# Kernel optimization log

Hardware: AMD Instinct MI355X
Metric: run time of the kernel (lower is better)

## Reference

```python
import jax, jax.numpy as jnp
import numpy as np

EPS = 1e-8

def _fft_unit_proj(x):
    # Project each vector to unit magnitude in the Fourier domain (norm_kv=True).
    f = jnp.fft.fft(x, axis=-1)
    return jnp.real(jnp.fft.ifft(f / (jnp.abs(f) + EPS), axis=-1))

def _hrr_key_value_query(k, v, q, causal=True):
    # k, v, q: [B, S, D]
    k = _fft_unit_proj(k)
    v = _fft_unit_proj(v)
    # bind: circular convolution of key and value
    kv = jnp.real(jnp.fft.ifft(jnp.fft.fft(k, axis=-1) * jnp.fft.fft(v, axis=-1), axis=-1))
    # causal associative memory: running sum of bound pairs along sequence
    if causal:
        mem = jnp.cumsum(kv, axis=1)
    else:
        mem = jnp.broadcast_to(jnp.sum(kv, axis=1, keepdims=True), kv.shape)
    # unbind: circular correlation of memory with query
    out = jnp.real(jnp.fft.ifft(jnp.conj(jnp.fft.fft(q, axis=-1)) * jnp.fft.fft(mem, axis=-1), axis=-1))
    return out


def setup_inputs() -> dict:
    key = jax.random.key(0)
    ks = jax.random.split(key, 8)
    B, S, D = 2, 4096, 2048
    sc = 1.0 / np.sqrt(D).astype(np.float32)
    return {
        "hidden_states": jax.random.normal(ks[0], (B, S, D), jnp.float32),
        "base_output": jax.random.normal(ks[1], (B, S, D), jnp.float32),
        "Wq": jax.random.normal(ks[2], (D, D), jnp.float32) * sc,
        "bq": jnp.zeros((D,), jnp.float32),
        "Wk": jax.random.normal(ks[3], (D, D), jnp.float32) * sc,
        "bk": jnp.zeros((D,), jnp.float32),
        "Wv": jax.random.normal(ks[4], (D, D), jnp.float32) * sc,
        "bv": jnp.zeros((D,), jnp.float32),
        "gate": jax.random.normal(ks[5], (1,), jnp.float32) * 0.1,
    }


def reference(hidden_states, base_output, Wq, bq, Wk, bk, Wv, bv, gate):
    # Adapter q/k/v projections (nn.Linear uses y = x @ W.T + b)
    q = jnp.einsum('bsd,ed->bse', hidden_states, Wq) + bq
    k = jnp.einsum('bsd,ed->bse', hidden_states, Wk) + bk
    v = jnp.einsum('bsd,ed->bse', hidden_states, Wv) + bv
    adapter = _hrr_key_value_query(k, v, q, causal=True)
    return base_output + gate * adapter
```

## Files before the change

### kernel.cpp

```cpp
#include <hip/hip_runtime.h>
#include <math.h>

constexpr int D_DIM  = 2048;
constexpr int HALF_D = 1024;
constexpr int B_DIM  = 2;
constexpr int S_DIM  = 4096;
constexpr int NROW   = B_DIM * S_DIM;
constexpr int NCHUNK = 64;
constexpr int CHLEN  = S_DIM / NCHUNK;
constexpr float EPS_ = 1e-8f;

typedef __attribute__((ext_vector_type(8))) short  short8;
typedef __attribute__((ext_vector_type(8))) unsigned short ushort8;
typedef __attribute__((ext_vector_type(4))) float  f32x4;

__device__ __forceinline__ float2 mkf2(float x, float y){ float2 r; r.x=x; r.y=y; return r; }
__device__ __forceinline__ float2 cmulf(float2 a, float2 b){
  return mkf2(fmaf(a.x, b.x, -a.y*b.y), fmaf(a.x, b.y, a.y*b.x));
}
__device__ __forceinline__ unsigned short f2bf(float x){
  unsigned u = __float_as_uint(x);
  u += 0x7fff + ((u >> 16) & 1);
  return (unsigned short)(u >> 16);
}
__device__ __forceinline__ float bf2f(unsigned short h){
  return __uint_as_float(((unsigned)h) << 16);
}

__global__ __launch_bounds__(256)
void cvt_f32_bf16(const float* __restrict__ in, unsigned short* __restrict__ out, int n8)
{
  int i = blockIdx.x * 256 + threadIdx.x;
  if (i >= n8) return;
  const float4* p = (const float4*)in + (size_t)i * 2;
  float4 a = p[0], b = p[1];
  ushort8 o;
  o[0]=f2bf(a.x); o[1]=f2bf(a.y); o[2]=f2bf(a.z); o[3]=f2bf(a.w);
  o[4]=f2bf(b.x); o[5]=f2bf(b.y); o[6]=f2bf(b.z); o[7]=f2bf(b.w);
  *(ushort8*)(out + (size_t)i * 8) = o;
}

__global__ __launch_bounds__(512, 2)
void gemm_fused(const unsigned short* __restrict__ A,
                const unsigned short* __restrict__ Wc,
                const float* __restrict__ bq, const float* __restrict__ bk,
                const float* __restrict__ bv,
                float* __restrict__ qout, unsigned short* __restrict__ kvb)
{
  constexpr int K = 2048, NT = K / 32;
  __shared__ unsigned short lds[49152];
  const int tid  = threadIdx.x;
  const int wid  = tid >> 6, lane = tid & 63;
  const int wr   = wid >> 2, wc = wid & 3;

  int bid = blockIdx.x;
  int sw  = (bid & 7) * 96 + (bid >> 3);
  const int bm = (sw / 24) * 256, bn = (sw % 24) * 256;

  const int srow = tid >> 2;
  const int skc  = ((tid & 3) ^ ((tid >> 3) & 3)) * 8;
  const unsigned short* Ag = A  + (size_t)(bm + srow) * K + skc;
  const unsigned short* Bg = Wc + (size_t)(bn + srow) * K + skc;

  unsigned short* Abase = lds;
  unsigned short* Bbase = lds + 24576;
  const int stoff = wid * 512;

  const int fr  = lane & 15;
  const int sig = ((lane >> 4) ^ ((lane >> 1) & 3)) * 8;
  const int aro = (wr * 128 + fr) * 32 + sig;
  const int bro = (wc * 64 + fr) * 32 + sig;

  auto stA = [&](int kt, int b, int r) {
    __builtin_amdgcn_global_load_lds(
      (const __attribute__((address_space(1))) void*)(Ag + (size_t)r * 128 * K + kt * 32),
      (__attribute__((address_space(3))) void*)(Abase + b * 8192 + r * 4096 + stoff),
      16, 0, 0);
  };
  auto stB = [&](int kt, int b, int r) {
    __builtin_amdgcn_global_load_lds(
      (const __attribute__((address_space(1))) void*)(Bg + (size_t)r * 128 * K + kt * 32),
      (__attribute__((address_space(3))) void*)(Bbase + b * 8192 + r * 4096 + stoff),
      16, 0, 0);
  };

  f32x4 acc[8][4];
#pragma unroll
  for (int i = 0; i < 8; ++i)
#pragma unroll
    for (int j = 0; j < 4; ++j) acc[i][j] = (f32x4){0.f, 0.f, 0.f, 0.f};

  stA(0, 0, 0); stA(0, 0, 1); stB(0, 0, 0); stB(0, 0, 1);
  stA(1, 1, 0); stA(1, 1, 1); stB(1, 1, 0); stB(1, 1, 1);
  asm volatile("s_waitcnt vmcnt(4)" ::: "memory");
  __builtin_amdgcn_s_barrier();
  __builtin_amdgcn_sched_barrier(0);

  int c = 0;
#pragma unroll 1
  for (int kt = 0; kt < NT; ++kt) {
    const unsigned short* Ab = Abase + c * 8192;
    const unsigned short* Bb = Bbase + c * 8192;
    int nb = c + 2; if (nb >= 3) nb -= 3;
    const bool st = (kt < NT - 2);

    if (st) { stA(kt + 2, nb, 0); stA(kt + 2, nb, 1); }
    short8 af0[4], bfr[4];
#pragma unroll
    for (int i = 0; i < 4; ++i) af0[i] = *(const short8*)(Ab + aro + i * 512);
#pragma unroll
    for (int j = 0; j < 4; ++j) bfr[j] = *(const short8*)(Bb + bro + j * 512);
    __builtin_amdgcn_s_barrier();
    asm volatile("s_waitcnt lgkmcnt(0)" ::: "memory");
    __builtin_amdgcn_sched_barrier(0);
    __builtin_amdgcn_s_setprio(1);
#pragma unroll
    for (int i = 0; i < 4; ++i)
#pragma unroll
      for (int j = 0; j < 4; ++j)
        acc[i][j] = __builtin_amdgcn_mfma_f32_16x16x32_bf16(af0[i], bfr[j], acc[i][j], 0, 0, 0);
    __builtin_amdgcn_s_setprio(0);
    __builtin_amdgcn_s_barrier();

    if (st) { stB(kt + 2, nb, 0); stB(kt + 2, nb, 1); }
    short8 af1[4];
#pragma unroll
    for (int i = 0; i < 4; ++i) af1[i] = *(const short8*)(Ab + aro + 2048 + i * 512);
    __builtin_amdgcn_s_barrier();
    asm volatile("s_waitcnt lgkmcnt(0)" ::: "memory");
    __builtin_amdgcn_sched_barrier(0);
    __builtin_amdgcn_s_setprio(1);
#pragma unroll
    for (int i = 0; i < 4; ++i)
#pragma unroll
      for (int j = 0; j < 4; ++j)
        acc[4 + i][j] = __builtin_amdgcn_mfma_f32_16x16x32_bf16(af1[i], bfr[j], acc[4 + i][j], 0, 0, 0);
    __builtin_amdgcn_s_setprio(0);
    if (st)                 asm volatile("s_waitcnt vmcnt(4)" ::: "memory");
    else if (kt == NT - 2)  asm volatile("s_waitcnt vmcnt(0)" ::: "memory");
    __builtin_amdgcn_s_barrier();
    c = (c == 2) ? 0 : c + 1;
  }

  const int seg = bn >> 11;
  const float* bp = (seg == 0) ? bq : (seg == 1) ? bk : bv;
  float bias_j[4];
#pragma unroll
  for (int j = 0; j < 4; ++j)
    bias_j[j] = bp[(bn + wc * 64 + j * 16 + fr) & 2047];
  const int er = (lane >> 4) * 4;
  const int kvoff = (seg == 2) ? 2048 : 0;
#pragma unroll
  for (int I = 0; I < 8; ++I) {
    int row = bm + wr * 128 + I * 16 + er;
#pragma unroll
    for (int j = 0; j < 4; ++j) {
      int col = (bn + wc * 64 + j * 16 + fr) & 2047;
#pragma unroll
      for (int r = 0; r < 4; ++r) {
        float val = acc[I][j][r] + bias_j[j];
        if (seg == 0)
          qout[(size_t)(row + r) * 2048 + col] = val;
        else
          kvb[(size_t)(row + r) * 4096 + kvoff + col] = f2bf(val);
      }
    }
  }
}

__device__ __forceinline__ int XS(int i){ return i ^ (((i >> 5) ^ (i >> 10)) & 31); }
__device__ __forceinline__ int TS(int i){ return i ^ ((i >> 5) & 31); }

__device__ __forceinline__ float2 mulmi(float2 w){ return mkf2(w.y, -w.x); }
__device__ __forceinline__ float2 mulw8(float2 w){
  const float c = 0.70710678118654752f;
  return mkf2(c * (w.x + w.y), c * (w.y - w.x));
}
__device__ __forceinline__ void bfly(float2& a, float2& b, float2 w){
  float2 v = cmulf(w, b);
  b = mkf2(a.x - v.x, a.y - v.y);
  a = mkf2(a.x + v.x, a.y + v.y);
}
__device__ __forceinline__ void bflyc(float2& a, float2& b, float2 w){
  float2 d = mkf2(a.x - b.x, a.y - b.y);
  a = mkf2(a.x + b.x, a.y + b.y);
  b = mkf2(fmaf(d.x, w.x, d.y * w.y), fmaf(d.y, w.x, -d.x * w.y));
}

__device__ __forceinline__ void fwd8(float2 e[8], float2 wA, float2 wB0, float2 wC0){
  bfly(e[0], e[1], wA); bfly(e[2], e[3], wA); bfly(e[4], e[5], wA); bfly(e[6], e[7], wA);
  float2 wB1 = mulmi(wB0);
  bfly(e[0], e[2], wB0); bfly(e[1], e[3], wB1); bfly(e[4], e[6], wB0); bfly(e[5], e[7], wB1);
  float2 wC1 = mulw8(wC0), wC2 = mulmi(wC0), wC3 = mulmi(wC1);
  bfly(e[0], e[4], wC0); bfly(e[1], e[5], wC1); bfly(e[2], e[6], wC2); bfly(e[3], e[7], wC3);
}
__device__ __forceinline__ void inv8(float2 e[8], float2 wA, float2 wB0, float2 wC0){
  float2 wC1 = mulw8(wC0), wC2 = mulmi(wC0), wC3 = mulmi(wC1);
  bflyc(e[0], e[4], wC0); bflyc(e[1], e[5], wC1); bflyc(e[2], e[6], wC2); bflyc(e[3], e[7], wC3);
  float2 wB1 = mulmi(wB0);
  bflyc(e[0], e[2], wB0); bflyc(e[1], e[3], wB1); bflyc(e[4], e[6], wB0); bflyc(e[5], e[7], wB1);
  bflyc(e[0], e[1], wA); bflyc(e[2], e[3], wA); bflyc(e[4], e[5], wA); bflyc(e[6], e[7], wA);
}

__device__ __forceinline__ float2 twld(const float* twr, const float* twi, int i){
  int s = TS(i);
  return mkf2(twr[s], twi[s]);
}

__device__ void fft_fwd(float2* X, const float* twr, const float* twi, int t)
{
  const float2 one = mkf2(1.f, 0.f);
  {
    int b = 8 * t;
    float2 e[8];
#pragma unroll
    for (int r = 0; r < 8; ++r) e[r] = X[XS(b + r)];
    fwd8(e, one, one, one);
#pragma unroll
    for (int r = 0; r < 8; ++r) X[XS(b + r)] = e[r];
  }
  __syncthreads();
  {
    int u = t >> 5, b = 64 * (t & 31) + u;
    float2 e[8];
#pragma unroll
    for (int r = 0; r < 8; ++r) e[r] = X[XS(b + 8 * r)];
    fwd8(e, twld(twr,twi,128*u), twld(twr,twi,64*u), twld(twr,twi,32*u));
#pragma unroll
    for (int r = 0; r < 8; ++r) X[XS(b + 8 * r)] = e[r];
  }
  __syncthreads();
  {
    int u = t & 63, b = 512 * (t >> 6) + u;
    float2 e[8];
#pragma unroll
    for (int r = 0; r < 8; ++r) e[r] = X[XS(b + 64 * r)];
    fwd8(e, twld(twr,twi,16*u), twld(twr,twi,8*u), twld(twr,twi,4*u));
#pragma unroll
    for (int r = 0; r < 8; ++r) X[XS(b + 64 * r)] = e[r];
  }
  __syncthreads();
#pragma unroll
  for (int h = 0; h < 2; ++h) {
    int u = t + 256 * h;
    float2 f[4];
#pragma unroll
    for (int r = 0; r < 4; ++r) f[r] = X[XS(u + 512 * r)];
    float2 wA = twld(twr,twi,2*u), wB0 = twld(twr,twi,u), wB1 = mulmi(wB0);
    bfly(f[0], f[1], wA);  bfly(f[2], f[3], wA);
    bfly(f[0], f[2], wB0); bfly(f[1], f[3], wB1);
#pragma unroll
    for (int r = 0; r < 4; ++r) X[XS(u + 512 * r)] = f[r];
  }
  __syncthreads();
}

__device__ void fft_inv(float2* X, const float* twr, const float* twi, int t)
{
  const float2 one = mkf2(1.f, 0.f);
#pragma unroll
  for (int h = 0; h < 2; ++h) {
    int u = t + 256 * h;
    float2 f[4];
#pragma unroll
    for (int r = 0; r < 4; ++r) f[r] = X[XS(u + 512 * r)];
    float2 wA = twld(twr,twi,2*u), wB0 = twld(twr,twi,u), wB1 = mulmi(wB0);
    bflyc(f[0], f[2], wB0); bflyc(f[1], f[3], wB1);
    bflyc(f[0], f[1], wA);  bflyc(f[2], f[3], wA);
#pragma unroll
    for (int r = 0; r < 4; ++r) X[XS(u + 512 * r)] = f[r];
  }
  __syncthreads();
  {
    int u = t & 63, b = 512 * (t >> 6) + u;
    float2 e[8];
#pragma unroll
    for (int r = 0; r < 8; ++r) e[r] = X[XS(b + 64 * r)];
    inv8(e, twld(twr,twi,16*u), twld(twr,twi,8*u), twld(twr,twi,4*u));
#pragma unroll
    for (int r = 0; r < 8; ++r) X[XS(b + 64 * r)] = e[r];
  }
  __syncthreads();
  {
    int u = t >> 5, b = 64 * (t & 31) + u;
    float2 e[8];
#pragma unroll
    for (int r = 0; r < 8; ++r) e[r] = X[XS(b + 8 * r)];
    inv8(e, twld(twr,twi,128*u), twld(twr,twi,64*u), twld(twr,twi,32*u));
#pragma unroll
    for (int r = 0; r < 8; ++r) X[XS(b + 8 * r)] = e[r];
  }
  __syncthreads();
  {
    int b = 8 * t;
    float2 e[8];
#pragma unroll
    for (int r = 0; r < 8; ++r) e[r] = X[XS(b + r)];
    inv8(e, one, one, one);
#pragma unroll
    for (int r = 0; r < 8; ++r) X[XS(b + r)] = e[r];
  }
  __syncthreads();
}

__global__ __launch_bounds__(256)
void twiddle_init(float2* __restrict__ twg)
{
  int i = blockIdx.x * 256 + threadIdx.x;
  if (i < HALF_D) {
    float sv, cv;
    sincosf(-6.283185307179586f * (float)i / (float)D_DIM, &sv, &cv);
    twg[i] = mkf2(cv, sv);
  }
}

__global__ __launch_bounds__(256)
void fftkv_kernel(unsigned short* __restrict__ kvb, const float2* __restrict__ twg)
{
  __shared__ float2 X[D_DIM];
  __shared__ float twr[HALF_D], twi[HALF_D];
  const int t = threadIdx.x;
  const size_t row = blockIdx.x;
  const unsigned short* kvrow = kvb + row * 4096;

  for (int i = t; i < HALF_D; i += 256) {
    float2 w = twg[i]; int s = TS(i); twr[s] = w.x; twi[s] = w.y;
  }
  for (int i = t; i < D_DIM; i += 256) {
    int p = __brev((unsigned)i) >> 21;
    X[XS(p)] = mkf2(bf2f(kvrow[i]), bf2f(kvrow[2048 + i]));
  }
  __syncthreads();
  fft_fwd(X, twr, twi, t);

  float2* outp = (float2*)(kvb + row * 4096);
  for (int d = t; d < HALF_D; d += 256) {
    float2 p;
    if (d == 0) {
      float2 z0 = X[XS(0)], zn = X[XS(HALF_D)];
      float k0 = z0.x, v0 = z0.y, kn = zn.x, vn = zn.y;
      float p0 = (k0 / (fabsf(k0) + EPS_)) * (v0 / (fabsf(v0) + EPS_));
      float pn = (kn / (fabsf(kn) + EPS_)) * (vn / (fabsf(vn) + EPS_));
      p = mkf2(p0, pn);
    } else {
      float2 A = X[XS(d)];
      float2 Bc = X[XS(D_DIM - d)];
      float2 Bj = mkf2(Bc.x, -Bc.y);
      float2 Fk = mkf2(0.5f * (A.x + Bj.x), 0.5f * (A.y + Bj.y));
      float2 tt = mkf2(0.5f * (A.x - Bj.x), 0.5f * (A.y - Bj.y));
      float2 Fv = mkf2(tt.y, -tt.x);
      float sa = 1.f / (sqrtf(Fk.x*Fk.x + Fk.y*Fk.y) + EPS_);
      float sb = 1.f / (sqrtf(Fv.x*Fv.x + Fv.y*Fv.y) + EPS_);
      p = cmulf(Fk, Fv);
      float sc = sa * sb;
      p.x *= sc; p.y *= sc;
    }
    outp[d] = p;
  }
}

__global__ __launch_bounds__(256)
void scan_partial(const float2* __restrict__ kv, float2* __restrict__ part)
{
  int gid = blockIdx.x * 256 + threadIdx.x;
  int d = gid & (HALF_D - 1);
  int chunk = (gid >> 10) & (NCHUNK - 1);
  int b = gid >> 16;
  const float2* p = kv + ((size_t)(b * S_DIM + chunk * CHLEN) * HALF_D) + d;
  float2 acc = mkf2(0.f, 0.f);
  for (int s = 0; s < CHLEN; ++s) {
    float2 v = p[(size_t)s * HALF_D];
    acc.x += v.x; acc.y += v.y;
  }
  part[gid] = acc;
}

__global__ __launch_bounds__(256)
void scan_offsets(float2* __restrict__ part)
{
  int gid = blockIdx.x * 256 + threadIdx.x;
  int d = gid & (HALF_D - 1);
  int b = gid >> 10;
  float2* p = part + (size_t)b * (NCHUNK * HALF_D) + d;
  float2 acc = mkf2(0.f, 0.f);
  for (int c = 0; c < NCHUNK; ++c) {
    float2 v = p[(size_t)c * HALF_D];
    p[(size_t)c * HALF_D] = acc;
    acc.x += v.x; acc.y += v.y;
  }
}

__global__ __launch_bounds__(256)
void scan_apply(float2* __restrict__ kv, const float2* __restrict__ part)
{
  int gid = blockIdx.x * 256 + threadIdx.x;
  int d = gid & (HALF_D - 1);
  int chunk = (gid >> 10) & (NCHUNK - 1);
  int b = gid >> 16;
  float2* p = kv + ((size_t)(b * S_DIM + chunk * CHLEN) * HALF_D) + d;
  float2 acc = part[gid];
  for (int s = 0; s < CHLEN; ++s) {
    float2 v = p[(size_t)s * HALF_D];
    acc.x += v.x; acc.y += v.y;
    p[(size_t)s * HALF_D] = acc;
  }
}

__global__ __launch_bounds__(256)
void final_kernel(float* __restrict__ qo, const float2* __restrict__ mem,
                  const float* __restrict__ base, const float* __restrict__ gate,
                  const float2* __restrict__ twg)
{
  __shared__ float2 X[D_DIM];
  __shared__ float twr[HALF_D], twi[HALF_D];
  const int t = threadIdx.x;
  const size_t row = blockIdx.x;
  float* qrow = qo + row * D_DIM;
  const float2* mrow = mem + row * HALF_D;

  for (int i = t; i < HALF_D; i += 256) {
    float2 w = twg[i]; int s = TS(i); twr[s] = w.x; twi[s] = w.y;
  }
  for (int i = t; i < D_DIM; i += 256) {
    int p = __brev((unsigned)i) >> 21;
    X[XS(p)] = mkf2(qrow[i], 0.f);
  }
  __syncthreads();
  fft_fwd(X, twr, twi, t);

  for (int d = t; d < HALF_D; d += 256) {
    if (d == 0) {
      float2 fm = mrow[0];
      float2 f0 = X[XS(0)], f1 = X[XS(HALF_D)];
      X[XS(0)]      = mkf2(f0.x * fm.x, -f0.y * fm.x);
      X[XS(HALF_D)] = mkf2(f1.x * fm.y, -f1.y * fm.y);
    } else {
      float2 fm = mrow[d];
      float2 fq = X[XS(d)];
      X[XS(d)] = mkf2(fq.x*fm.x + fq.y*fm.y, fq.x*fm.y - fq.y*fm.x);
      float2 f2 = X[XS(D_DIM - d)];
      X[XS(D_DIM - d)] = mkf2(f2.x*fm.x - f2.y*fm.y, -f2.x*fm.y - f2.y*fm.x);
    }
  }
  __syncthreads();
  fft_inv(X, twr, twi, t);

  const float gv = gate[0] * (1.f / (float)D_DIM);
  const float* brow = base + row * D_DIM;
  for (int i = t; i < D_DIM; i += 256) {
    int p = __brev((unsigned)i) >> 21;
    qrow[i] = brow[i] + gv * X[XS(p)].x;
  }
}

extern "C" void kernel_launch(void* const* d_in, const int* in_sizes, int n_in,
                              void* d_out, int out_size, void* d_ws, size_t ws_size,
                              hipStream_t stream)
{
  const float* hs   = (const float*)d_in[0];
  const float* base = (const float*)d_in[1];
  const float* Wq   = (const float*)d_in[2];
  const float* bq   = (const float*)d_in[3];
  const float* Wk   = (const float*)d_in[4];
  const float* bk   = (const float*)d_in[5];
  const float* Wv   = (const float*)d_in[6];
  const float* bv   = (const float*)d_in[7];
  const float* gate = (const float*)d_in[8];
  float* out  = (float*)d_out;

  char* ws = (char*)d_ws;
  unsigned short* hsb = (unsigned short*)ws;
  unsigned short* wqb = (unsigned short*)(ws + 33554432);
  unsigned short* wkb = wqb + (size_t)D_DIM * D_DIM;
  unsigned short* wvb = wkb + (size_t)D_DIM * D_DIM;
  unsigned short* kvb = (unsigned short*)(ws + 58720256);
  float2* part = (float2*)(ws + 58720256 + 67108864);
  float2* twg  = (float2*)ws;

  {
    int n8 = (NROW * D_DIM) / 8;
    cvt_f32_bf16<<<n8 / 256, 256, 0, stream>>>(hs, hsb, n8);
    int w8 = (D_DIM * D_DIM) / 8;
    cvt_f32_bf16<<<w8 / 256, 256, 0, stream>>>(Wq, wqb, w8);
    cvt_f32_bf16<<<w8 / 256, 256, 0, stream>>>(Wk, wkb, w8);
    cvt_f32_bf16<<<w8 / 256, 256, 0, stream>>>(Wv, wvb, w8);
  }

  gemm_fused<<<768, 512, 0, stream>>>(hsb, wqb, bq, bk, bv, out, kvb);

  twiddle_init<<<4, 256, 0, stream>>>(twg);

  fftkv_kernel<<<NROW, 256, 0, stream>>>(kvb, twg);

  scan_partial<<<(B_DIM * NCHUNK * HALF_D) / 256, 256, 0, stream>>>(
      (const float2*)kvb, part);
  scan_offsets<<<(B_DIM * HALF_D) / 256, 256, 0, stream>>>(part);
  scan_apply<<<(B_DIM * NCHUNK * HALF_D) / 256, 256, 0, stream>>>(
      (float2*)kvb, part);

  final_kernel<<<NROW, 256, 0, stream>>>(out, (const float2*)kvb, base, gate, twg);
}
```

Measured before the change: 433.3 us.

## Store q and frequency-domain kv in bf16, vectorize scans, retile GEMM to 256x128

The GEMM now writes q as bf16 instead of fp32. The fftkv kernel packs its complex spectrum output into bf16 pairs. The scan and final kernels read and write these bf16 buffers with 16-byte vectorized accesses and fp32 accumulators. The GEMM is retiled from 256x256 blocks of 512 threads to 256x128 blocks of 256 threads, with the LDS staging resized to match. The aim is to halve intermediate memory traffic in the bandwidth-bound scan and FFT stages, but the running-sum memory rounded to bf16 adds accuracy risk, and the scan kernels now launch only 128 blocks.

Result: faster. 404.4 us (-6.7%).

```diff
diff --git a/kernel.cpp b/kernel.cpp
--- a/kernel.cpp
+++ b/kernel.cpp
@@ -40,22 +40,22 @@
   *(ushort8*)(out + (size_t)i * 8) = o;
 }
 
-__global__ __launch_bounds__(512, 2)
+__global__ __launch_bounds__(256, 2)
 void gemm_fused(const unsigned short* __restrict__ A,
                 const unsigned short* __restrict__ Wc,
                 const float* __restrict__ bq, const float* __restrict__ bk,
                 const float* __restrict__ bv,
-                float* __restrict__ qout, unsigned short* __restrict__ kvb)
+                unsigned short* __restrict__ qb, unsigned short* __restrict__ kvb)
 {
   constexpr int K = 2048, NT = K / 32;
-  __shared__ unsigned short lds[49152];
+  __shared__ unsigned short lds[36864];
   const int tid  = threadIdx.x;
   const int wid  = tid >> 6, lane = tid & 63;
-  const int wr   = wid >> 2, wc = wid & 3;
+  const int wr   = wid >> 1, wc = wid & 1;
 
   int bid = blockIdx.x;
-  int sw  = (bid & 7) * 96 + (bid >> 3);
-  const int bm = (sw / 24) * 256, bn = (sw % 24) * 256;
+  int sw  = (bid & 7) * 192 + (bid >> 3);
+  const int bm = (sw / 48) * 256, bn = (sw % 48) * 128;
 
   const int srow = tid >> 2;
   const int skc  = ((tid & 3) ^ ((tid >> 3) & 3)) * 8;
@@ -73,14 +73,14 @@
 
   auto stA = [&](int kt, int b, int r) {
     __builtin_amdgcn_global_load_lds(
-      (const __attribute__((address_space(1))) void*)(Ag + (size_t)r * 128 * K + kt * 32),
-      (__attribute__((address_space(3))) void*)(Abase + b * 8192 + r * 4096 + stoff),
+      (const __attribute__((address_space(1))) void*)(Ag + (size_t)r * 64 * K + kt * 32),
+      (__attribute__((address_space(3))) void*)(Abase + b * 8192 + r * 2048 + stoff),
       16, 0, 0);
   };
   auto stB = [&](int kt, int b, int r) {
     __builtin_amdgcn_global_load_lds(
-      (const __attribute__((address_space(1))) void*)(Bg + (size_t)r * 128 * K + kt * 32),
-      (__attribute__((address_space(3))) void*)(Bbase + b * 8192 + r * 4096 + stoff),
+      (const __attribute__((address_space(1))) void*)(Bg + (size_t)r * 64 * K + kt * 32),
+      (__attribute__((address_space(3))) void*)(Bbase + b * 4096 + r * 2048 + stoff),
       16, 0, 0);
   };
 
@@ -90,9 +90,9 @@
 #pragma unroll
     for (int j = 0; j < 4; ++j) acc[i][j] = (f32x4){0.f, 0.f, 0.f, 0.f};
 
-  stA(0, 0, 0); stA(0, 0, 1); stB(0, 0, 0); stB(0, 0, 1);
-  stA(1, 1, 0); stA(1, 1, 1); stB(1, 1, 0); stB(1, 1, 1);
-  asm volatile("s_waitcnt vmcnt(4)" ::: "memory");
+  stA(0, 0, 0); stA(0, 0, 1); stA(0, 0, 2); stA(0, 0, 3); stB(0, 0, 0); stB(0, 0, 1);
+  stA(1, 1, 0); stA(1, 1, 1); stA(1, 1, 2); stA(1, 1, 3); stB(1, 1, 0); stB(1, 1, 1);
+  asm volatile("s_waitcnt vmcnt(6)" ::: "memory");
   __builtin_amdgcn_s_barrier();
   __builtin_amdgcn_sched_barrier(0);
 
@@ -100,11 +100,11 @@
 #pragma unroll 1
   for (int kt = 0; kt < NT; ++kt) {
     const unsigned short* Ab = Abase + c * 8192;
-    const unsigned short* Bb = Bbase + c * 8192;
+    const unsigned short* Bb = Bbase + c * 4096;
     int nb = c + 2; if (nb >= 3) nb -= 3;
     const bool st = (kt < NT - 2);
 
-    if (st) { stA(kt + 2, nb, 0); stA(kt + 2, nb, 1); }
+    if (st) { stA(kt + 2, nb, 0); stA(kt + 2, nb, 1); stA(kt + 2, nb, 2); stA(kt + 2, nb, 3); }
     short8 af0[4], bfr[4];
 #pragma unroll
     for (int i = 0; i < 4; ++i) af0[i] = *(const short8*)(Ab + aro + i * 512);
@@ -136,7 +136,7 @@
       for (int j = 0; j < 4; ++j)
         acc[4 + i][j] = __builtin_amdgcn_mfma_f32_16x16x32_bf16(af1[i], bfr[j], acc[4 + i][j], 0, 0, 0);
     __builtin_amdgcn_s_setprio(0);
-    if (st)                 asm volatile("s_waitcnt vmcnt(4)" ::: "memory");
+    if (st)                 asm volatile("s_waitcnt vmcnt(6)" ::: "memory");
     else if (kt == NT - 2)  asm volatile("s_waitcnt vmcnt(0)" ::: "memory");
     __builtin_amdgcn_s_barrier();
     c = (c == 2) ? 0 : c + 1;
@@ -149,7 +149,9 @@
   for (int j = 0; j < 4; ++j)
     bias_j[j] = bp[(bn + wc * 64 + j * 16 + fr) & 2047];
   const int er = (lane >> 4) * 4;
-  const int kvoff = (seg == 2) ? 2048 : 0;
+  unsigned short* dst = (seg == 0) ? qb : kvb;
+  const size_t rstride = (seg == 0) ? 2048 : 4096;
+  const int coff = (seg == 2) ? 2048 : 0;
 #pragma unroll
   for (int I = 0; I < 8; ++I) {
     int row = bm + wr * 128 + I * 16 + er;
@@ -159,10 +161,7 @@
 #pragma unroll
       for (int r = 0; r < 4; ++r) {
         float val = acc[I][j][r] + bias_j[j];
-        if (seg == 0)
-          qout[(size_t)(row + r) * 2048 + col] = val;
-        else
-          kvb[(size_t)(row + r) * 4096 + kvoff + col] = f2bf(val);
+        dst[(size_t)(row + r) * rstride + coff + col] = f2bf(val);
       }
     }
   }
@@ -326,14 +325,21 @@
   for (int i = t; i < HALF_D; i += 256) {
     float2 w = twg[i]; int s = TS(i); twr[s] = w.x; twi[s] = w.y;
   }
-  for (int i = t; i < D_DIM; i += 256) {
-    int p = __brev((unsigned)i) >> 21;
-    X[XS(p)] = mkf2(bf2f(kvrow[i]), bf2f(kvrow[2048 + i]));
+  {
+    int i0 = t * 8;
+    ushort8 k8 = *(const ushort8*)(kvrow + i0);
+    ushort8 v8 = *(const ushort8*)(kvrow + 2048 + i0);
+#pragma unroll
+    for (int r = 0; r < 8; ++r) {
+      int i = i0 + r;
+      int p = __brev((unsigned)i) >> 21;
+      X[XS(p)] = mkf2(bf2f(k8[r]), bf2f(v8[r]));
+    }
   }
   __syncthreads();
   fft_fwd(X, twr, twi, t);
 
-  float2* outp = (float2*)(kvb + row * 4096);
+  unsigned int* outp = (unsigned int*)(kvb + row * 4096);
   for (int d = t; d < HALF_D; d += 256) {
     float2 p;
     if (d == 0) {
@@ -355,24 +361,27 @@
       float sc = sa * sb;
       p.x *= sc; p.y *= sc;
     }
-    outp[d] = p;
-  }
-}
-
-__global__ __launch_bounds__(256)
-void scan_partial(const float2* __restrict__ kv, float2* __restrict__ part)
+    outp[d] = (unsigned)f2bf(p.x) | ((unsigned)f2bf(p.y) << 16);
+  }
+}
+
+__global__ __launch_bounds__(256)
+void scan_partial(const unsigned short* __restrict__ kvb, float2* __restrict__ part)
 {
   int gid = blockIdx.x * 256 + threadIdx.x;
-  int d = gid & (HALF_D - 1);
-  int chunk = (gid >> 10) & (NCHUNK - 1);
-  int b = gid >> 16;
-  const float2* p = kv + ((size_t)(b * S_DIM + chunk * CHLEN) * HALF_D) + d;
-  float2 acc = mkf2(0.f, 0.f);
+  int q4 = gid & 255;
+  int chunk = (gid >> 8) & (NCHUNK - 1);
+  int b = gid >> 14;
+  const unsigned short* p = kvb + (size_t)(b * S_DIM + chunk * CHLEN) * 4096 + q4 * 8;
+  float ar[4] = {0,0,0,0}, ai[4] = {0,0,0,0};
   for (int s = 0; s < CHLEN; ++s) {
-    float2 v = p[(size_t)s * HALF_D];
-    acc.x += v.x; acc.y += v.y;
-  }
-  part[gid] = acc;
+    ushort8 v = *(const ushort8*)(p + (size_t)s * 4096);
+#pragma unroll
+    for (int e = 0; e < 4; ++e) { ar[e] += bf2f(v[2*e]); ai[e] += bf2f(v[2*e+1]); }
+  }
+  float2* pp = part + (size_t)(b * NCHUNK + chunk) * HALF_D + q4 * 4;
+#pragma unroll
+  for (int e = 0; e < 4; ++e) pp[e] = mkf2(ar[e], ai[e]);
 }
 
 __global__ __launch_bounds__(256)
@@ -391,65 +400,80 @@
 }
 
 __global__ __launch_bounds__(256)
-void scan_apply(float2* __restrict__ kv, const float2* __restrict__ part)
+void scan_apply(unsigned short* __restrict__ kvb, const float2* __restrict__ part)
 {
   int gid = blockIdx.x * 256 + threadIdx.x;
-  int d = gid & (HALF_D - 1);
-  int chunk = (gid >> 10) & (NCHUNK - 1);
-  int b = gid >> 16;
-  float2* p = kv + ((size_t)(b * S_DIM + chunk * CHLEN) * HALF_D) + d;
-  float2 acc = part[gid];
+  int q4 = gid & 255;
+  int chunk = (gid >> 8) & (NCHUNK - 1);
+  int b = gid >> 14;
+  unsigned short* p = kvb + (size_t)(b * S_DIM + chunk * CHLEN) * 4096 + q4 * 8;
+  const float2* pp = part + (size_t)(b * NCHUNK + chunk) * HALF_D + q4 * 4;
+  float ar[4], ai[4];
+#pragma unroll
+  for (int e = 0; e < 4; ++e) { float2 v = pp[e]; ar[e] = v.x; ai[e] = v.y; }
   for (int s = 0; s < CHLEN; ++s) {
-    float2 v = p[(size_t)s * HALF_D];
-    acc.x += v.x; acc.y += v.y;
-    p[(size_t)s * HALF_D] = acc;
-  }
-}
-
-__global__ __launch_bounds__(256)
-void final_kernel(float* __restrict__ qo, const float2* __restrict__ mem,
+    ushort8 v = *(const ushort8*)(p + (size_t)s * 4096);
+    ushort8 o;
+#pragma unroll
+    for (int e = 0; e < 4; ++e) {
+      ar[e] += bf2f(v[2*e]); ai[e] += bf2f(v[2*e+1]);
+      o[2*e] = f2bf(ar[e]); o[2*e+1] = f2bf(ai[e]);
+    }
+    *(ushort8*)(p + (size_t)s * 4096) = o;
+  }
+}
+
+__global__ __launch_bounds__(256)
+void final_kernel(const unsigned short* __restrict__ qb,
+                  const unsigned short* __restrict__ kvb,
                   const float* __restrict__ base, const float* __restrict__ gate,
-                  const float2* __restrict__ twg)
+                  const float2* __restrict__ twg, float* __restrict__ out)
 {
   __shared__ float2 X[D_DIM];
   __shared__ float twr[HALF_D], twi[HALF_D];
   const int t = threadIdx.x;
   const size_t row = blockIdx.x;
-  float* qrow = qo + row * D_DIM;
-  const float2* mrow = mem + row * HALF_D;
+  const unsigned short* qrow = qb + row * 2048;
+  const unsigned short* mrow = kvb + row * 4096;
 
   for (int i = t; i < HALF_D; i += 256) {
     float2 w = twg[i]; int s = TS(i); twr[s] = w.x; twi[s] = w.y;
   }
+  {
+    int i0 = t * 8;
+    ushort8 q8 = *(const ushort8*)(qrow + i0);
+#pragma unroll
+    for (int r = 0; r < 8; ++r) {
+      int i = i0 + r;
+      int p = __brev((unsigned)i) >> 21;
+      X[XS(p)] = mkf2(bf2f(q8[r]), 0.f);
+    }
+  }
+  __syncthreads();
+  fft_fwd(X, twr, twi, t);
+
+  for (int d = t; d < HALF_D; d += 256) {
+    float fmre = bf2f(mrow[2*d]), fmim = bf2f(mrow[2*d+1]);
+    if (d == 0) {
+      float2 f0 = X[XS(0)], f1 = X[XS(HALF_D)];
+      X[XS(0)]      = mkf2(f0.x * fmre, -f0.y * fmre);
+      X[XS(HALF_D)] = mkf2(f1.x * fmim, -f1.y * fmim);
+    } else {
+      float2 fq = X[XS(d)];
+      X[XS(d)] = mkf2(fq.x*fmre + fq.y*fmim, fq.x*fmim - fq.y*fmre);
+      float2 f2 = X[XS(D_DIM - d)];
+      X[XS(D_DIM - d)] = mkf2(f2.x*fmre - f2.y*fmim, -f2.x*fmim - f2.y*fmre);
+    }
+  }
+  __syncthreads();
+  fft_inv(X, twr, twi, t);
+
+  const float gv = gate[0] * (1.f / (float)D_DIM);
+  const float* brow = base + row * D_DIM;
+  float* orow = out + row * D_DIM;
   for (int i = t; i < D_DIM; i += 256) {
     int p = __brev((unsigned)i) >> 21;
-    X[XS(p)] = mkf2(qrow[i], 0.f);
-  }
-  __syncthreads();
-  fft_fwd(X, twr, twi, t);
-
-  for (int d = t; d < HALF_D; d += 256) {
-    if (d == 0) {
-      float2 fm = mrow[0];
-      float2 f0 = X[XS(0)], f1 = X[XS(HALF_D)];
-      X[XS(0)]      = mkf2(f0.x * fm.x, -f0.y * fm.x);
-      X[XS(HALF_D)] = mkf2(f1.x * fm.y, -f1.y * fm.y);
-    } else {
-      float2 fm = mrow[d];
-      float2 fq = X[XS(d)];
-      X[XS(d)] = mkf2(fq.x*fm.x + fq.y*fm.y, fq.x*fm.y - fq.y*fm.x);
-      float2 f2 = X[XS(D_DIM - d)];
-      X[XS(D_DIM - d)] = mkf2(f2.x*fm.x - f2.y*fm.y, -f2.x*fm.y - f2.y*fm.x);
-    }
-  }
-  __syncthreads();
-  fft_inv(X, twr, twi, t);
-
-  const float gv = gate[0] * (1.f / (float)D_DIM);
-  const float* brow = base + row * D_DIM;
-  for (int i = t; i < D_DIM; i += 256) {
-    int p = __brev((unsigned)i) >> 21;
-    qrow[i] = brow[i] + gv * X[XS(p)].x;
+    orow[i] = brow[i] + gv * X[XS(p)].x;
   }
 }
 
@@ -474,7 +498,8 @@
   unsigned short* wkb = wqb + (size_t)D_DIM * D_DIM;
   unsigned short* wvb = wkb + (size_t)D_DIM * D_DIM;
   unsigned short* kvb = (unsigned short*)(ws + 58720256);
-  float2* part = (float2*)(ws + 58720256 + 67108864);
+  unsigned short* qb  = (unsigned short*)(ws + 58720256 + 67108864);
+  float2* part = (float2*)(ws + 58720256 + 67108864 + 33554432);
   float2* twg  = (float2*)ws;
 
   {
@@ -486,17 +511,15 @@
     cvt_f32_bf16<<<w8 / 256, 256, 0, stream>>>(Wv, wvb, w8);
   }
 
-  gemm_fused<<<768, 512, 0, stream>>>(hsb, wqb, bq, bk, bv, out, kvb);
+  gemm_fused<<<1536, 256, 0, stream>>>(hsb, wqb, bq, bk, bv, qb, kvb);
 
   twiddle_init<<<4, 256, 0, stream>>>(twg);
 
   fftkv_kernel<<<NROW, 256, 0, stream>>>(kvb, twg);
 
-  scan_partial<<<(B_DIM * NCHUNK * HALF_D) / 256, 256, 0, stream>>>(
-      (const float2*)kvb, part);
+  scan_partial<<<128, 256, 0, stream>>>(kvb, part);
   scan_offsets<<<(B_DIM * HALF_D) / 256, 256, 0, stream>>>(part);
-  scan_apply<<<(B_DIM * NCHUNK * HALF_D) / 256, 256, 0, stream>>>(
-      (float2*)kvb, part);
-
-  final_kernel<<<NROW, 256, 0, stream>>>(out, (const float2*)kvb, base, gate, twg);
-}
+  scan_apply<<<128, 256, 0, stream>>>(kvb, part);
+
+  final_kernel<<<NROW, 256, 0, stream>>>(qb, kvb, base, gate, twg, out);
+}
```
